# Kernel optimization log

Hardware: AMD Instinct MI355X
Metric: run time of the kernel (lower is better)

Reference implementation:

```python
import jax, jax.numpy as jnp
import numpy as np

N_HEAD, D_HEAD, D_MODEL = 16, 64, 1024
QLEN, MEM_LEN, BSZ = 1024, 1024, 2
KLEN = QLEN + MEM_LEN  # 2048; rlen == klen
LN_EPS = 1e-5


def _rel_shift(x):
    # x: [qlen, rlen, bsz, n_head] -- Transformer-XL pad/reshape trick
    q, r, b, n = x.shape
    pad = jnp.ones((q, 1, b, n), dtype=x.dtype)
    xp = jnp.concatenate([pad, x], axis=1)          # [q, r+1, b, n]
    xp = xp.reshape(r + 1, q, b, n)                  # reinterpret contiguous buffer
    return xp[1:].reshape(q, r, b, n)


def _layer_norm(x, g, b):
    mu = jnp.mean(x, axis=-1, keepdims=True)
    var = jnp.var(x, axis=-1, keepdims=True)
    return (x - mu) * jax.lax.rsqrt(var + LN_EPS) * g + b


def setup_inputs() -> dict:
    key = jax.random.key(0)
    ks = jax.random.split(key, 8)
    s = 0.02
    w = jax.random.normal(ks[0], (QLEN, BSZ, D_MODEL), jnp.float32)
    r = jax.random.normal(ks[1], (KLEN, D_MODEL), jnp.float32)
    r_w_bias = jax.random.normal(ks[2], (N_HEAD, D_HEAD), jnp.float32) * s
    r_r_bias = jax.random.normal(ks[3], (N_HEAD, D_HEAD), jnp.float32) * s
    mems = jax.random.normal(ks[4], (MEM_LEN, BSZ, D_MODEL), jnp.float32)
    qkv_W = jax.random.normal(ks[5], (3 * N_HEAD * D_HEAD, D_MODEL), jnp.float32) * s
    r_W = jax.random.normal(ks[6], (N_HEAD * D_HEAD, D_MODEL), jnp.float32) * s
    o_W = jax.random.normal(ks[7], (D_MODEL, N_HEAD * D_HEAD), jnp.float32) * s
    ln_g = jnp.ones((D_MODEL,), jnp.float32)
    ln_b = jnp.zeros((D_MODEL,), jnp.float32)
    # causal mask with memory: query i may attend keys j <= i + mem_len
    i = jnp.arange(QLEN)[:, None]
    j = jnp.arange(KLEN)[None, :]
    attn_mask = jnp.broadcast_to((j > i + MEM_LEN)[:, :, None], (QLEN, KLEN, BSZ))
    return {"w": w, "r": r, "r_w_bias": r_w_bias, "r_r_bias": r_r_bias,
            "mems": mems, "attn_mask": attn_mask, "qkv_W": qkv_W, "r_W": r_W,
            "o_W": o_W, "ln_g": ln_g, "ln_b": ln_b}


def reference(w, r, r_w_bias, r_r_bias, mems, attn_mask, qkv_W, r_W, o_W, ln_g, ln_b):
    qlen, bsz, _ = w.shape
    rlen = r.shape[0]
    scale = 1.0 / (D_HEAD ** 0.5)

    cat = jnp.concatenate([mems, w], axis=0)                 # [klen, b, d_model]
    w_heads = cat @ qkv_W.T                                  # [klen, b, 3*n*d]
    r_head_k = (r @ r_W.T).reshape(rlen, N_HEAD, D_HEAD)     # [rlen, n, d]

    w_head_q, w_head_k, w_head_v = jnp.split(w_heads, 3, axis=-1)
    w_head_q = w_head_q[-qlen:]
    klen = w_head_k.shape[0]

    w_head_q = w_head_q.reshape(qlen, bsz, N_HEAD, D_HEAD)
    w_head_k = w_head_k.reshape(klen, bsz, N_HEAD, D_HEAD)
    w_head_v = w_head_v.reshape(klen, bsz, N_HEAD, D_HEAD)

    AC = jnp.einsum('ibnd,jbnd->ijbn', w_head_q + r_w_bias, w_head_k)
    BD = jnp.einsum('ibnd,jnd->ijbn', w_head_q + r_r_bias, r_head_k)
    BD = _rel_shift(BD)

    attn_score = (AC + BD) * scale                            # [q, k, b, n]
    attn_score = jnp.where(attn_mask[:, :, :, None], -jnp.inf, attn_score)
    attn_prob = jax.nn.softmax(attn_score, axis=1)

    attn_vec = jnp.einsum('ijbn,jbnd->ibnd', attn_prob, w_head_v)
    attn_vec = attn_vec.reshape(qlen, bsz, N_HEAD * D_HEAD)
    attn_out = attn_vec @ o_W.T
    return _layer_norm(w + attn_out, ln_g, ln_b)
```

## Files before the change

kernel.cpp:

```cpp
#include <hip/hip_runtime.h>


typedef __attribute__((ext_vector_type(8))) short short8;
typedef __attribute__((ext_vector_type(4))) float f32x4;

#define AS1C(p) ((const __attribute__((address_space(1))) void*)(p))
#define AS3(p)  ((__attribute__((address_space(3))) void*)(p))

__device__ __forceinline__ f32x4 mfma16(short8 a, short8 b, f32x4 c) {
  return __builtin_amdgcn_mfma_f32_16x16x32_bf16(a, b, c, 0, 0, 0);
}

__device__ __forceinline__ unsigned short f2bf(float x) {
  union { float f; unsigned int u; } v; v.f = x;
  unsigned int r = v.u + 0x7fffu + ((v.u >> 16) & 1u);
  return (unsigned short)(r >> 16);
}
__device__ __forceinline__ float bf2f(unsigned short x) {
  union { unsigned int u; float f; } v; v.u = ((unsigned int)x) << 16;
  return v.f;
}
__device__ __forceinline__ f32x4 f4zero() {
  f32x4 z = {0.f, 0.f, 0.f, 0.f};
  return z;
}

__global__ __launch_bounds__(256) void k_conv(const float* __restrict__ src,
                                              unsigned short* __restrict__ dst) {
  size_t i = ((size_t)blockIdx.x * 256 + threadIdx.x) * 4;
  float4 v = *(const float4*)(src + i);
  unsigned int lo = (unsigned int)f2bf(v.x) | ((unsigned int)f2bf(v.y) << 16);
  unsigned int hi = (unsigned int)f2bf(v.z) | ((unsigned int)f2bf(v.w) << 16);
  uint2 o; o.x = lo; o.y = hi;
  *(uint2*)(dst + i) = o;
}

__device__ __forceinline__ void gemm_core(const unsigned short* __restrict__ A,
                                          const unsigned short* __restrict__ B,
                                          int m0, int n0,
                                          unsigned short* As, unsigned short* Bs,
                                          f32x4 (&acc)[4][4]) {
  const int tid = threadIdx.x;
  const int lane = tid & 63;
  const int w = tid >> 6;
  const int wm = (w >> 1) * 64, wn = (w & 1) * 64;
  const int l15 = lane & 15, lg = lane >> 4;
#pragma unroll
  for (int mi = 0; mi < 4; ++mi)
#pragma unroll
    for (int ni = 0; ni < 4; ++ni) acc[mi][ni] = f4zero();

  const int o = tid * 16;
  const int row0 = o >> 6;
  const int col0 = (o >> 1) & 31;
  const int ldst = o >> 1;

  for (int kt = 0; kt < 1024; kt += 32) {
    __syncthreads();
#pragma unroll
    for (int u = 0; u < 2; ++u) {
      __builtin_amdgcn_global_load_lds(
          AS1C(A + (size_t)(m0 + row0 + u * 64) * 1024 + kt + col0),
          AS3(As + ldst + u * 2048), 16, 0, 0);
      __builtin_amdgcn_global_load_lds(
          AS1C(B + (size_t)(n0 + row0 + u * 64) * 1024 + kt + col0),
          AS3(Bs + ldst + u * 2048), 16, 0, 0);
    }
    __syncthreads();
    short8 af[4], bfv[4];
#pragma unroll
    for (int mi = 0; mi < 4; ++mi)
      af[mi] = *(const short8*)&As[(wm + mi * 16 + l15) * 32 + lg * 8];
#pragma unroll
    for (int ni = 0; ni < 4; ++ni)
      bfv[ni] = *(const short8*)&Bs[(wn + ni * 16 + l15) * 32 + lg * 8];
#pragma unroll
    for (int mi = 0; mi < 4; ++mi)
#pragma unroll
      for (int ni = 0; ni < 4; ++ni)
        acc[mi][ni] = mfma16(af[mi], bfv[ni], acc[mi][ni]);
  }
}

__global__ __launch_bounds__(256) void k_gemm_qkv(
    const unsigned short* __restrict__ A, const unsigned short* __restrict__ B,
    unsigned short* __restrict__ Qrw, unsigned short* __restrict__ Qrr,
    unsigned short* __restrict__ Kd, unsigned short* __restrict__ Vd,
    const float* __restrict__ rwb, const float* __restrict__ rrb) {
  __shared__ unsigned short As[4096], Bs[4096];
  f32x4 acc[4][4];
  const int m0 = blockIdx.y * 128, n0 = blockIdx.x * 128;
  gemm_core(A, B, m0, n0, As, Bs, acc);
  const int tid = threadIdx.x, lane = tid & 63, w = tid >> 6;
  const int wm = (w >> 1) * 64, wn = (w & 1) * 64;
  const int l15 = lane & 15, lg = lane >> 4;
#pragma unroll
  for (int mi = 0; mi < 4; ++mi)
#pragma unroll
    for (int ni = 0; ni < 4; ++ni)
#pragma unroll
      for (int r = 0; r < 4; ++r) {
        float v = acc[mi][ni][r];
        int gm = m0 + wm + mi * 16 + lg * 4 + r;
        int gn = n0 + wn + ni * 16 + l15;
        int t = gm >> 1, b = gm & 1;
        if (gn < 1024) {
          if (t >= 1024) {
            int i = t - 1024;
            int hn = gn >> 6, d = gn & 63;
            size_t off = (((size_t)(b * 16 + hn)) * 1024 + i) * 64 + d;
            Qrw[off] = f2bf(v + rwb[gn]);
            Qrr[off] = f2bf(v + rrb[gn]);
          }
        } else if (gn < 2048) {
          int c = gn - 1024, hn = c >> 6, d = c & 63;
          Kd[(((size_t)(b * 16 + hn)) * 2048 + t) * 64 + d] = f2bf(v);
        } else {
          int c = gn - 2048, hn = c >> 6, d = c & 63;
          Vd[(((size_t)(b * 16 + hn)) * 2048 + t) * 64 + d] = f2bf(v);
        }
      }
}

__global__ __launch_bounds__(256) void k_gemm_rk(
    const unsigned short* __restrict__ A, const unsigned short* __restrict__ B,
    unsigned short* __restrict__ RKd) {
  __shared__ unsigned short As[4096], Bs[4096];
  f32x4 acc[4][4];
  const int m0 = blockIdx.y * 128, n0 = blockIdx.x * 128;
  gemm_core(A, B, m0, n0, As, Bs, acc);
  const int tid = threadIdx.x, lane = tid & 63, w = tid >> 6;
  const int wm = (w >> 1) * 64, wn = (w & 1) * 64;
  const int l15 = lane & 15, lg = lane >> 4;
#pragma unroll
  for (int mi = 0; mi < 4; ++mi)
#pragma unroll
    for (int ni = 0; ni < 4; ++ni)
#pragma unroll
      for (int r = 0; r < 4; ++r) {
        int gm = m0 + wm + mi * 16 + lg * 4 + r;
        int gn = n0 + wn + ni * 16 + l15;
        int hn = gn >> 6, d = gn & 63;
        RKd[(((size_t)hn) * 2048 + gm) * 64 + d] = f2bf(acc[mi][ni][r]);
      }
}

__global__ __launch_bounds__(256) void k_gemm_o(
    const unsigned short* __restrict__ A, const unsigned short* __restrict__ B,
    float* __restrict__ AO) {
  __shared__ unsigned short As[4096], Bs[4096];
  f32x4 acc[4][4];
  const int m0 = blockIdx.y * 128, n0 = blockIdx.x * 128;
  gemm_core(A, B, m0, n0, As, Bs, acc);
  const int tid = threadIdx.x, lane = tid & 63, w = tid >> 6;
  const int wm = (w >> 1) * 64, wn = (w & 1) * 64;
  const int l15 = lane & 15, lg = lane >> 4;
#pragma unroll
  for (int mi = 0; mi < 4; ++mi)
#pragma unroll
    for (int ni = 0; ni < 4; ++ni)
#pragma unroll
      for (int r = 0; r < 4; ++r) {
        int gm = m0 + wm + mi * 16 + lg * 4 + r;
        int gn = n0 + wn + ni * 16 + l15;
        AO[(size_t)gm * 1024 + gn] = acc[mi][ni][r];
      }
}

__global__ __launch_bounds__(256, 2) void k_attn(
    const unsigned short* __restrict__ Qrw, const unsigned short* __restrict__ Qrr,
    const unsigned short* __restrict__ Kd, const unsigned short* __restrict__ Vd,
    const unsigned short* __restrict__ RKd, unsigned short* __restrict__ AV) {
  __shared__ unsigned short Qrw_s[64][72], Qrr_s[64][72];
  __shared__ unsigned short KP_s[64][72];
  __shared__ unsigned short Vt_s[64][72];
  __shared__ unsigned short RK_s[128][72];
  __shared__ unsigned short BD_s[64][132];

  const int it = blockIdx.x, bn = blockIdx.y;
  const int b = bn >> 4, hn = bn & 15;
  const int i0 = it * 64;
  const int tid = threadIdx.x, lane = tid & 63, w = tid >> 6;
  const int l15 = lane & 15, lg = lane >> 4;
  const int istrip = w * 16;

  {
    const size_t qbase = (((size_t)(b * 16 + hn)) * 1024 + i0) * 64;
#pragma unroll
    for (int u = 0; u < 2; ++u) {
      int c = tid + u * 256;
      int row = c >> 3, col = (c & 7) * 8;
      *(short8*)&Qrw_s[row][col] = *(const short8*)&Qrw[qbase + row * 64 + col];
      *(short8*)&Qrr_s[row][col] = *(const short8*)&Qrr[qbase + row * 64 + col];
    }
  }

  float m_st[4], l_st[4];
  f32x4 accO[4];
#pragma unroll
  for (int r = 0; r < 4; ++r) { m_st[r] = -1e30f; l_st[r] = 0.f; }
#pragma unroll
  for (int df = 0; df < 4; ++df) accO[df] = f4zero();

  const size_t kvbase = ((size_t)(b * 16 + hn)) * 2048 * 64;
  const int njt = it + 17;

  for (int jt = 0; jt < njt; ++jt) {
    const int j0 = jt * 64;
    __syncthreads();
#pragma unroll
    for (int u = 0; u < 2; ++u) {
      int c = tid + u * 256;
      int row = c >> 3, col = (c & 7) * 8;
      *(short8*)&KP_s[row][col] = *(const short8*)&Kd[kvbase + (size_t)(j0 + row) * 64 + col];
      short8 vv = *(const short8*)&Vd[kvbase + (size_t)(j0 + row) * 64 + col];
#pragma unroll
      for (int e = 0; e < 8; ++e) Vt_s[col + e][row] = (unsigned short)vv[e];
    }
    const int jrb = j0 + 960 - i0;
#pragma unroll
    for (int u = 0; u < 4; ++u) {
      int c = tid + u * 256;
      int row = c >> 3, col = (c & 7) * 8;
      int jr = jrb + row;
      jr = jr < 0 ? 0 : (jr > 2047 ? 2047 : jr);
      *(short8*)&RK_s[row][col] = *(const short8*)&RKd[((size_t)hn * 2048 + jr) * 64 + col];
    }
    __syncthreads();

    f32x4 accS[4];
#pragma unroll
    for (int ni = 0; ni < 4; ++ni) accS[ni] = f4zero();
#pragma unroll
    for (int kk = 0; kk < 2; ++kk) {
      short8 aq = *(const short8*)&Qrw_s[istrip + l15][kk * 32 + lg * 8];
#pragma unroll
      for (int ni = 0; ni < 4; ++ni) {
        short8 bk = *(const short8*)&KP_s[ni * 16 + l15][kk * 32 + lg * 8];
        accS[ni] = mfma16(aq, bk, accS[ni]);
      }
    }
    f32x4 accB[8];
#pragma unroll
    for (int fi = 0; fi < 8; ++fi) accB[fi] = f4zero();
#pragma unroll
    for (int kk = 0; kk < 2; ++kk) {
      short8 aq = *(const short8*)&Qrr_s[istrip + l15][kk * 32 + lg * 8];
#pragma unroll
      for (int fi = 0; fi < 8; ++fi) {
        short8 br = *(const short8*)&RK_s[fi * 16 + l15][kk * 32 + lg * 8];
        accB[fi] = mfma16(aq, br, accB[fi]);
      }
    }
#pragma unroll
    for (int fi = 0; fi < 8; ++fi)
#pragma unroll
      for (int r = 0; r < 4; ++r)
        BD_s[istrip + lg * 4 + r][fi * 16 + l15] = f2bf(accB[fi][r]);
    __syncthreads();

    float p[4][4], mx[4];
#pragma unroll
    for (int r = 0; r < 4; ++r) mx[r] = -1e30f;
#pragma unroll
    for (int ni = 0; ni < 4; ++ni) {
      const int tj = ni * 16 + l15;
      const int gj = j0 + tj;
#pragma unroll
      for (int r = 0; r < 4; ++r) {
        const int ti = istrip + lg * 4 + r;
        const int gi = i0 + ti;
        float s = accS[ni][r] + bf2f(BD_s[ti][tj - ti + 63]);
        s = (gj <= gi + 1024) ? s * 0.125f : -1e30f;
        p[ni][r] = s;
        mx[r] = fmaxf(mx[r], s);
      }
    }
#pragma unroll
    for (int off = 1; off < 16; off <<= 1)
#pragma unroll
      for (int r = 0; r < 4; ++r) mx[r] = fmaxf(mx[r], __shfl_xor(mx[r], off));
    float rs[4], rowsum[4];
#pragma unroll
    for (int r = 0; r < 4; ++r) {
      float mnew = fmaxf(m_st[r], mx[r]);
      rs[r] = __expf(m_st[r] - mnew);
      m_st[r] = mnew;
      rowsum[r] = 0.f;
    }
#pragma unroll
    for (int ni = 0; ni < 4; ++ni)
#pragma unroll
      for (int r = 0; r < 4; ++r) {
        float e = __expf(p[ni][r] - m_st[r]);
        p[ni][r] = e;
        rowsum[r] += e;
      }
#pragma unroll
    for (int off = 1; off < 16; off <<= 1)
#pragma unroll
      for (int r = 0; r < 4; ++r) rowsum[r] += __shfl_xor(rowsum[r], off);
#pragma unroll
    for (int r = 0; r < 4; ++r) l_st[r] = l_st[r] * rs[r] + rowsum[r];
#pragma unroll
    for (int df = 0; df < 4; ++df) {
      f32x4 t = accO[df];
#pragma unroll
      for (int r = 0; r < 4; ++r) t[r] *= rs[r];
      accO[df] = t;
    }
#pragma unroll
    for (int ni = 0; ni < 4; ++ni)
#pragma unroll
      for (int r = 0; r < 4; ++r)
        KP_s[istrip + lg * 4 + r][ni * 16 + l15] = f2bf(p[ni][r]);
#pragma unroll
    for (int kk = 0; kk < 2; ++kk) {
      short8 ap = *(const short8*)&KP_s[istrip + l15][kk * 32 + lg * 8];
#pragma unroll
      for (int df = 0; df < 4; ++df) {
        short8 bv = *(const short8*)&Vt_s[df * 16 + l15][kk * 32 + lg * 8];
        accO[df] = mfma16(ap, bv, accO[df]);
      }
    }
  }
#pragma unroll
  for (int df = 0; df < 4; ++df)
#pragma unroll
    for (int r = 0; r < 4; ++r) {
      int ti = istrip + lg * 4 + r;
      int gi = i0 + ti;
      int d = df * 16 + l15;
      float v = accO[df][r] / l_st[r];
      AV[((size_t)gi * 2 + b) * 1024 + hn * 64 + d] = f2bf(v);
    }
}

__global__ __launch_bounds__(256) void k_ln(const float* __restrict__ wres,
                                            const float* __restrict__ ao,
                                            const float* __restrict__ g,
                                            const float* __restrict__ bb,
                                            float* __restrict__ out) {
  const int row = blockIdx.x;
  const int t4 = threadIdx.x * 4;
  const float4 xv = *(const float4*)(wres + (size_t)row * 1024 + t4);
  const float4 av = *(const float4*)(ao + (size_t)row * 1024 + t4);
  float x0 = xv.x + av.x, x1 = xv.y + av.y, x2 = xv.z + av.z, x3 = xv.w + av.w;
  float s1 = x0 + x1 + x2 + x3;
  float s2 = x0 * x0 + x1 * x1 + x2 * x2 + x3 * x3;
#pragma unroll
  for (int off = 1; off < 64; off <<= 1) {
    s1 += __shfl_xor(s1, off);
    s2 += __shfl_xor(s2, off);
  }
  __shared__ float red[2][4];
  const int wv = threadIdx.x >> 6;
  if ((threadIdx.x & 63) == 0) { red[0][wv] = s1; red[1][wv] = s2; }
  __syncthreads();
  s1 = red[0][0] + red[0][1] + red[0][2] + red[0][3];
  s2 = red[1][0] + red[1][1] + red[1][2] + red[1][3];
  const float mu = s1 * (1.f / 1024.f);
  const float var = s2 * (1.f / 1024.f) - mu * mu;
  const float inv = rsqrtf(var + 1e-5f);
  const float4 gv = *(const float4*)(g + t4);
  const float4 bv = *(const float4*)(bb + t4);
  float4 ov;
  ov.x = (x0 - mu) * inv * gv.x + bv.x;
  ov.y = (x1 - mu) * inv * gv.y + bv.y;
  ov.z = (x2 - mu) * inv * gv.z + bv.z;
  ov.w = (x3 - mu) * inv * gv.w + bv.w;
  *(float4*)(out + (size_t)row * 1024 + t4) = ov;
}

extern "C" void kernel_launch(void* const* d_in, const int* in_sizes, int n_in,
                              void* d_out, int out_size, void* d_ws, size_t ws_size,
                              hipStream_t stream) {
  const float* w     = (const float*)d_in[0];
  const float* r     = (const float*)d_in[1];
  const float* rwb   = (const float*)d_in[2];
  const float* rrb   = (const float*)d_in[3];
  const float* mems  = (const float*)d_in[4];
  const float* qkv_W = (const float*)d_in[6];
  const float* r_W   = (const float*)d_in[7];
  const float* o_W   = (const float*)d_in[8];
  const float* ln_g  = (const float*)d_in[9];
  const float* ln_b  = (const float*)d_in[10];
  float* out = (float*)d_out;
  char* ws = (char*)d_ws;

  unsigned short* A_cat = (unsigned short*)(ws + 0);
  unsigned short* Wqkv  = (unsigned short*)(ws + 8388608);
  unsigned short* rb    = (unsigned short*)(ws + 14680064);
  unsigned short* Wr    = (unsigned short*)(ws + 18874368);
  unsigned short* oWb   = (unsigned short*)(ws + 20971520);
  unsigned short* Qrw   = (unsigned short*)(ws + 23068672);
  unsigned short* Qrr   = (unsigned short*)(ws + 27262976);
  unsigned short* Kd    = (unsigned short*)(ws + 31457280);
  unsigned short* Vd    = (unsigned short*)(ws + 39845888);
  unsigned short* RKd   = (unsigned short*)(ws + 48234496);
  unsigned short* AV    = (unsigned short*)(ws + 52428800);
  float*          AO    = (float*)(ws + 56623104);

  k_conv<<<2048, 256, 0, stream>>>(mems, A_cat);
  k_conv<<<2048, 256, 0, stream>>>(w, A_cat + 2048 * 1024);
  k_conv<<<3072, 256, 0, stream>>>(qkv_W, Wqkv);
  k_conv<<<2048, 256, 0, stream>>>(r, rb);
  k_conv<<<1024, 256, 0, stream>>>(r_W, Wr);
  k_conv<<<1024, 256, 0, stream>>>(o_W, oWb);

  k_gemm_qkv<<<dim3(24, 32), 256, 0, stream>>>(A_cat, Wqkv, Qrw, Qrr, Kd, Vd, rwb, rrb);
  k_gemm_rk<<<dim3(8, 16), 256, 0, stream>>>(rb, Wr, RKd);
  k_attn<<<dim3(16, 32), 256, 0, stream>>>(Qrw, Qrr, Kd, Vd, RKd, AV);
  k_gemm_o<<<dim3(8, 16), 256, 0, stream>>>(AV, oWb, AO);
  k_ln<<<2048, 256, 0, stream>>>(w, AO, ln_g, ln_b, out);
}
```

Before: 360.8 us.

## Fuse conversion launches, keep Q in registers, swizzle V tile, raise attention occupancy

The six fp32-to-bf16 conversion launches become one kernel that picks its source and destination by block index, which removes per-launch overhead. In the attention kernel, the Q fragments are loaded straight into registers instead of shared memory, and the transposed V tile gets an XOR swizzle so the scattered transpose writes and the MFMA reads cause fewer LDS bank conflicts. Shared memory drops as a result, and launch bounds rise to 3 blocks per CU for more occupancy. The risk is register pressure and spilling under the tighter register limit.

```diff
diff --git a/kernel.cpp b/kernel.cpp
--- a/kernel.cpp
+++ b/kernel.cpp
@@ -25,9 +25,22 @@
   return z;
 }
 
-__global__ __launch_bounds__(256) void k_conv(const float* __restrict__ src,
-                                              unsigned short* __restrict__ dst) {
-  size_t i = ((size_t)blockIdx.x * 256 + threadIdx.x) * 4;
+__global__ __launch_bounds__(256) void k_conv_all(
+    const float* __restrict__ s0, const float* __restrict__ s1,
+    const float* __restrict__ s2, const float* __restrict__ s3,
+    const float* __restrict__ s4, const float* __restrict__ s5,
+    unsigned short* __restrict__ d0, unsigned short* __restrict__ d1,
+    unsigned short* __restrict__ d2, unsigned short* __restrict__ d3,
+    unsigned short* __restrict__ d4, unsigned short* __restrict__ d5) {
+  int b = blockIdx.x;
+  const float* src; unsigned short* dst; int off;
+  if (b < 2048)       { src = s0; dst = d0; off = b; }
+  else if (b < 4096)  { src = s1; dst = d1; off = b - 2048; }
+  else if (b < 7168)  { src = s2; dst = d2; off = b - 4096; }
+  else if (b < 9216)  { src = s3; dst = d3; off = b - 7168; }
+  else if (b < 10240) { src = s4; dst = d4; off = b - 9216; }
+  else                { src = s5; dst = d5; off = b - 10240; }
+  size_t i = ((size_t)off * 256 + threadIdx.x) * 4;
   float4 v = *(const float4*)(src + i);
   unsigned int lo = (unsigned int)f2bf(v.x) | ((unsigned int)f2bf(v.y) << 16);
   unsigned int hi = (unsigned int)f2bf(v.z) | ((unsigned int)f2bf(v.w) << 16);
@@ -167,15 +180,14 @@
       }
 }
 
-__global__ __launch_bounds__(256, 2) void k_attn(
+__global__ __launch_bounds__(256, 3) void k_attn(
     const unsigned short* __restrict__ Qrw, const unsigned short* __restrict__ Qrr,
     const unsigned short* __restrict__ Kd, const unsigned short* __restrict__ Vd,
     const unsigned short* __restrict__ RKd, unsigned short* __restrict__ AV) {
-  __shared__ unsigned short Qrw_s[64][72], Qrr_s[64][72];
-  __shared__ unsigned short KP_s[64][72];
-  __shared__ unsigned short Vt_s[64][72];
-  __shared__ unsigned short RK_s[128][72];
-  __shared__ unsigned short BD_s[64][132];
+  __shared__ __attribute__((aligned(16))) unsigned short KP_s[64][72];
+  __shared__ __attribute__((aligned(16))) unsigned short Vt_s[64][64];
+  __shared__ __attribute__((aligned(16))) unsigned short RK_s[128][72];
+  __shared__ __attribute__((aligned(16))) unsigned short BD_s[64][130];
 
   const int it = blockIdx.x, bn = blockIdx.y;
   const int b = bn >> 4, hn = bn & 15;
@@ -184,15 +196,13 @@
   const int l15 = lane & 15, lg = lane >> 4;
   const int istrip = w * 16;
 
+  short8 qrw_r[2], qrr_r[2];
   {
-    const size_t qbase = (((size_t)(b * 16 + hn)) * 1024 + i0) * 64;
-#pragma unroll
-    for (int u = 0; u < 2; ++u) {
-      int c = tid + u * 256;
-      int row = c >> 3, col = (c & 7) * 8;
-      *(short8*)&Qrw_s[row][col] = *(const short8*)&Qrw[qbase + row * 64 + col];
-      *(short8*)&Qrr_s[row][col] = *(const short8*)&Qrr[qbase + row * 64 + col];
-    }
+    const size_t qrow = (((size_t)(b * 16 + hn)) * 1024 + i0 + istrip + l15) * 64 + lg * 8;
+    qrw_r[0] = *(const short8*)&Qrw[qrow];
+    qrw_r[1] = *(const short8*)&Qrw[qrow + 32];
+    qrr_r[0] = *(const short8*)&Qrr[qrow];
+    qrr_r[1] = *(const short8*)&Qrr[qrow + 32];
   }
 
   float m_st[4], l_st[4];
@@ -214,8 +224,12 @@
       int row = c >> 3, col = (c & 7) * 8;
       *(short8*)&KP_s[row][col] = *(const short8*)&Kd[kvbase + (size_t)(j0 + row) * 64 + col];
       short8 vv = *(const short8*)&Vd[kvbase + (size_t)(j0 + row) * 64 + col];
-#pragma unroll
-      for (int e = 0; e < 8; ++e) Vt_s[col + e][row] = (unsigned short)vv[e];
+      const int grow = row >> 3, jo = row & 7;
+#pragma unroll
+      for (int e = 0; e < 8; ++e) {
+        int d = col + e;
+        Vt_s[d][((grow ^ (d >> 3)) << 3) + jo] = (unsigned short)vv[e];
+      }
     }
     const int jrb = j0 + 960 - i0;
 #pragma unroll
@@ -233,11 +247,10 @@
     for (int ni = 0; ni < 4; ++ni) accS[ni] = f4zero();
 #pragma unroll
     for (int kk = 0; kk < 2; ++kk) {
-      short8 aq = *(const short8*)&Qrw_s[istrip + l15][kk * 32 + lg * 8];
 #pragma unroll
       for (int ni = 0; ni < 4; ++ni) {
         short8 bk = *(const short8*)&KP_s[ni * 16 + l15][kk * 32 + lg * 8];
-        accS[ni] = mfma16(aq, bk, accS[ni]);
+        accS[ni] = mfma16(qrw_r[kk], bk, accS[ni]);
       }
     }
     f32x4 accB[8];
@@ -245,11 +258,10 @@
     for (int fi = 0; fi < 8; ++fi) accB[fi] = f4zero();
 #pragma unroll
     for (int kk = 0; kk < 2; ++kk) {
-      short8 aq = *(const short8*)&Qrr_s[istrip + l15][kk * 32 + lg * 8];
 #pragma unroll
       for (int fi = 0; fi < 8; ++fi) {
         short8 br = *(const short8*)&RK_s[fi * 16 + l15][kk * 32 + lg * 8];
-        accB[fi] = mfma16(aq, br, accB[fi]);
+        accB[fi] = mfma16(qrr_r[kk], br, accB[fi]);
       }
     }
 #pragma unroll
@@ -319,7 +331,8 @@
       short8 ap = *(const short8*)&KP_s[istrip + l15][kk * 32 + lg * 8];
 #pragma unroll
       for (int df = 0; df < 4; ++df) {
-        short8 bv = *(const short8*)&Vt_s[df * 16 + l15][kk * 32 + lg * 8];
+        const int dr = df * 16 + l15;
+        short8 bv = *(const short8*)&Vt_s[dr][((kk * 4 + lg) ^ ((dr >> 3) & 7)) << 3];
         accO[df] = mfma16(ap, bv, accO[df]);
       }
     }
@@ -401,12 +414,8 @@
   unsigned short* AV    = (unsigned short*)(ws + 52428800);
   float*          AO    = (float*)(ws + 56623104);
 
-  k_conv<<<2048, 256, 0, stream>>>(mems, A_cat);
-  k_conv<<<2048, 256, 0, stream>>>(w, A_cat + 2048 * 1024);
-  k_conv<<<3072, 256, 0, stream>>>(qkv_W, Wqkv);
-  k_conv<<<2048, 256, 0, stream>>>(r, rb);
-  k_conv<<<1024, 256, 0, stream>>>(r_W, Wr);
-  k_conv<<<1024, 256, 0, stream>>>(o_W, oWb);
+  k_conv_all<<<11264, 256, 0, stream>>>(mems, w, qkv_W, r, r_W, o_W,
+                                        A_cat, A_cat + 2048 * 1024, Wqkv, rb, Wr, oWb);
 
   k_gemm_qkv<<<dim3(24, 32), 256, 0, stream>>>(A_cat, Wqkv, Qrw, Qrr, Kd, Vd, rwb, rrb);
   k_gemm_rk<<<dim3(8, 16), 256, 0, stream>>>(rb, Wr, RKd);
```

After: 354.4 us. No clear change (-1.8%).
